# Kernel tuning notes

Hardware: AMD Instinct MI355X
Metric: run time of the kernel (lower is better)

## Reference

```python
import jax, jax.numpy as jnp
import numpy as np

B, E, H, W, P, C = 2, 256, 192, 192, 16, 80
GRIDS = (40, 36, 24, 16, 12)
L = len(GRIDS)
MASK_W, CLS_W, ALPHA, GAMMA, EPS = 3.0, 1.0, 0.25, 2.0, 1e-4


def setup_inputs() -> dict:
    key = jax.random.key(0)
    ks = jax.random.split(key, 32)
    inp = {"mask_out": jax.random.normal(ks[0], (B, E, H, W), jnp.float32)}
    for i, g in enumerate(GRIDS):
        inp[f"kernel_l{i}"] = jax.random.normal(ks[1 + i], (B, g, g, E), jnp.float32) * 0.05
        inp[f"cate_l{i}"] = jax.random.uniform(ks[6 + i], (B, g, g, C), jnp.float32)
        inp[f"pos_l{i}"] = jax.random.randint(ks[11 + i], (B, P), 0, g * g, dtype=jnp.int32)
        inp[f"cate_t_l{i}"] = jax.random.randint(ks[16 + i], (B, g, g), -1, C, dtype=jnp.int32)
    # binary instance masks, image-major layout [B, L, P, H, W]
    inp["mask_targets"] = (jax.random.uniform(ks[21], (B, L, P, H, W)) > 0.9).astype(jnp.float32)
    return inp


def _forward(mask_out, kernels, cates, mask_targets, pos_idxs, cate_ts):
    # --- dynamic 1x1 conv: gather positive kernels and apply as batched matmul ---
    preds = []
    for kl, pl in zip(kernels, pos_idxs):
        g2 = kl.shape[1] * kl.shape[2]
        kflat = kl.reshape(B, g2, E)
        kp = jnp.take_along_axis(kflat, pl[:, :, None], axis=1)  # [B, P, E]
        preds.append(jnp.einsum('bpe,behw->bphw', kp, mask_out))  # F.conv2d 1x1
    preds = jnp.stack(preds)  # [L, B, P, H, W]  (level-major, matches torch cat order)

    # --- dice loss ---
    mp = jax.nn.sigmoid(preds).reshape(L * B * P, H * W)
    # NOTE: original code concatenates targets image-major (img, level) while preds
    # are level-major (level, img); we reproduce that pairing faithfully.
    mt = mask_targets.reshape(B * L * P, H * W)
    a = jnp.sum(mp * mt, axis=1)
    b = jnp.sum(mp * mp, axis=1)
    c = jnp.sum(mt * mt, axis=1)
    mask_loss = jnp.sum(1.0 - 2.0 * a / (b + c + 1e-4)) / (L * B * P)

    # --- focal loss on positive grid cells ---
    tgt = jnp.concatenate([t.reshape(-1) for t in cate_ts])            # [N]
    prd = jnp.concatenate([cl.reshape(-1, C) for cl in cates])          # [N, C]
    posm = (tgt > -1).astype(jnp.float32)
    p = jnp.clip(prd, EPS, 1.0 - EPS)
    gt = jax.nn.one_hot(jnp.clip(tgt, 0, C - 1), C, dtype=jnp.float32)
    af = jnp.where(gt == 1.0, ALPHA, 1.0 - ALPHA)
    pt = jnp.where(gt == 1.0, p, 1.0 - p)
    fw = af * (1.0 - pt) ** GAMMA
    ce = -(gt * jnp.log(p) + (1.0 - gt) * jnp.log(1.0 - p))
    cls_loss = jnp.sum(fw * ce * posm[:, None]) / jnp.sum(posm)

    return jnp.stack([MASK_W * mask_loss, CLS_W * cls_loss])  # [mask_loss, cls_loss]


def reference(mask_out, kernel_l0, kernel_l1, kernel_l2, kernel_l3, kernel_l4,
              cate_l0, cate_l1, cate_l2, cate_l3, cate_l4, mask_targets,
              pos_l0, pos_l1, pos_l2, pos_l3, pos_l4,
              cate_t_l0, cate_t_l1, cate_t_l2, cate_t_l3, cate_t_l4):
    return _forward(mask_out,
                    (kernel_l0, kernel_l1, kernel_l2, kernel_l3, kernel_l4),
                    (cate_l0, cate_l1, cate_l2, cate_l3, cate_l4),
                    mask_targets,
                    (pos_l0, pos_l1, pos_l2, pos_l3, pos_l4),
                    (cate_t_l0, cate_t_l1, cate_t_l2, cate_t_l3, cate_t_l4))
```

## Files before the change

### kernel.cpp

```cpp
#include <hip/hip_runtime.h>
#include <hip/hip_bf16.h>

namespace {

constexpr int kHW = 36864;

typedef __attribute__((ext_vector_type(8))) short bf16x8;
typedef __attribute__((ext_vector_type(4))) float f32x4;

__device__ __forceinline__ unsigned short f2bf(float x) {
  return __builtin_bit_cast(unsigned short, __float2bfloat16(x));
}
__device__ __forceinline__ float bf2f(unsigned short u) {
  return __builtin_bit_cast(float, (unsigned int)u << 16);
}

__device__ __forceinline__ float wave_sum(float v) {
#pragma unroll
  for (int off = 32; off; off >>= 1) v += __shfl_xor(v, off, 64);
  return v;
}

__global__ __launch_bounds__(256) void prep_kernel(
    const float* __restrict__ k0, const float* __restrict__ k1,
    const float* __restrict__ k2, const float* __restrict__ k3,
    const float* __restrict__ k4,
    const int* __restrict__ q0, const int* __restrict__ q1,
    const int* __restrict__ q2, const int* __restrict__ q3,
    const int* __restrict__ q4,
    unsigned short* __restrict__ kbf, float* __restrict__ acc) {
  const int bid = blockIdx.x;
  if (bid == 0) {
    for (int i = threadIdx.x; i < 482; i += 256) acc[i] = 0.f;
    return;
  }
  const int idx = bid - 1;
  const int b = idx / 80;
  const int row = idx - b * 80;
  if (threadIdx.x >= 128) return;
  const int l = row >> 4, p = row & 15;
  const float* kb[5] = {k0, k1, k2, k3, k4};
  const int* pb[5] = {q0, q1, q2, q3, q4};
  const int bg2[5] = {b * 1600, b * 1296, b * 576, b * 256, b * 144};
  const int pos = pb[l][b * 16 + p];
  const int ch = threadIdx.x * 2;
  const float2 kv = *(const float2*)(kb[l] + (size_t)(bg2[l] + pos) * 256 + ch);
  *(unsigned int*)&kbf[((size_t)b * 80 + row) * 256 + ch] =
      (unsigned int)f2bf(kv.x) | ((unsigned int)f2bf(kv.y) << 16);
}

template <int FUSED>
__global__ __launch_bounds__(256, 4) void gemm_kernel(
    const float* __restrict__ mask_out,
    const unsigned short* __restrict__ kbf,
    const float* __restrict__ mask_targets,
    unsigned short* __restrict__ predw,
    float* __restrict__ acc) {
  __shared__ float bufB[2][32][64];
  __shared__ float bred[4][240];

  const int bid = blockIdx.x;
  const int b = bid / 576;
  const int tile = bid - b * 576;
  const int px0 = tile * 64;
  const int lane = threadIdx.x & 63;
  const int wv = threadIdx.x >> 6;
  const int px16 = lane & 15;
  const int hi8 = (lane >> 4) * 8;
  const int pxl = px0 + wv * 16 + px16;

  const unsigned short* __restrict__ ka =
      kbf + ((size_t)b * 80 + px16) * 256 + hi8;

  const float* __restrict__ gstage = mask_out + (size_t)b * 256 * kHW +
                                     (size_t)(wv * 4 + (lane >> 4)) * kHW +
                                     px0 + (lane & 15) * 4;

#define STAGE(CUR, KS)                                                       \
  {                                                                          \
    const float* gs = gstage + (size_t)(KS)*32 * kHW;                        \
    __builtin_amdgcn_global_load_lds(                                        \
        (const __attribute__((address_space(1))) unsigned int*)gs,           \
        (__attribute__((address_space(3))) unsigned int*)&bufB[CUR][wv * 4]  \
            [0],                                                             \
        16, 0, 0);                                                           \
    __builtin_amdgcn_global_load_lds(                                        \
        (const __attribute__((address_space(1))) unsigned int*)(gs +         \
                                                                16 * kHW),   \
        (__attribute__((address_space(3))) unsigned int*)&bufB[CUR][wv * 4 + \
                                                                   16][0],   \
        16, 0, 0);                                                           \
  }

  f32x4 a5[5];
#pragma unroll
  for (int mt = 0; mt < 5; ++mt) a5[mt] = (f32x4){0.f, 0.f, 0.f, 0.f};

  STAGE(0, 0);
  __syncthreads();

#pragma unroll
  for (int ks = 0; ks < 8; ++ks) {
    if (ks + 1 < 8) STAGE((ks + 1) & 1, ks + 1);
    float fb[8];
#pragma unroll
    for (int j = 0; j < 8; ++j) fb[j] = bufB[ks & 1][hi8 + j][wv * 16 + px16];
    bf16x8 bb;
#pragma unroll
    for (int j = 0; j < 8; ++j) bb[j] = (short)f2bf(fb[j]);
#pragma unroll
    for (int mt = 0; mt < 5; ++mt) {
      const bf16x8 af = *(const bf16x8*)(ka + mt * 4096 + ks * 32);
      a5[mt] =
          __builtin_amdgcn_mfma_f32_16x16x32_bf16(af, bb, a5[mt], 0, 0, 0);
    }
    __syncthreads();
  }
#undef STAGE

  if constexpr (FUSED == 0) {
#pragma unroll
    for (int mt = 0; mt < 5; ++mt) {
#pragma unroll
      for (int j = 0; j < 4; ++j) {
        const int row80 = mt * 16 + (lane >> 4) * 4 + j;
        const int r = (row80 >> 4) * 32 + b * 16 + (row80 & 15);
        predw[(size_t)r * kHW + pxl] = f2bf(a5[mt][j]);
      }
    }
  } else {
#pragma unroll
    for (int mt = 0; mt < 5; ++mt) {
#pragma unroll
      for (int j = 0; j < 4; ++j) {
        const int row80 = mt * 16 + (lane >> 4) * 4 + j;
        const int r = (row80 >> 4) * 32 + b * 16 + (row80 & 15);
        const float mp = 1.f / (1.f + __expf(-a5[mt][j]));
        const float tv = mask_targets[(size_t)r * kHW + pxl];
        float av = mp * tv;
        float bv = mp * mp;
        float cv = tv;
#pragma unroll
        for (int m = 1; m <= 8; m <<= 1) {
          av += __shfl_xor(av, m, 64);
          bv += __shfl_xor(bv, m, 64);
          cv += __shfl_xor(cv, m, 64);
        }
        if (px16 == 0) {
          bred[wv][row80] = av;
          bred[wv][80 + row80] = bv;
          bred[wv][160 + row80] = cv;
        }
      }
    }
    __syncthreads();
    if (threadIdx.x < 240) {
      const int q = threadIdx.x / 80;
      const int row80 = threadIdx.x - q * 80;
      const int r = (row80 >> 4) * 32 + b * 16 + (row80 & 15);
      const float s = bred[0][threadIdx.x] + bred[1][threadIdx.x] +
                      bred[2][threadIdx.x] + bred[3][threadIdx.x];
      unsafeAtomicAdd(&acc[q * 160 + r], s);
    }
  }
}

__global__ __launch_bounds__(256) void dice_kernel(
    const unsigned short* __restrict__ predw,
    const float* __restrict__ mtg, float* __restrict__ acc) {
  const int r = blockIdx.x / 18;
  const int cb = blockIdx.x - r * 18;
  const int px = cb * 2048 + threadIdx.x * 8;
  const size_t base = (size_t)r * kHW + px;
  const bf16x8 p8 = *(const bf16x8*)&predw[base];
  const float4 t0 = *(const float4*)&mtg[base];
  const float4 t1 = *(const float4*)&mtg[base + 4];
  const float tv[8] = {t0.x, t0.y, t0.z, t0.w, t1.x, t1.y, t1.z, t1.w};
  float av = 0.f, bv = 0.f, cv = 0.f;
#pragma unroll
  for (int j = 0; j < 8; ++j) {
    const float x = bf2f((unsigned short)p8[j]);
    const float mp = 1.f / (1.f + __expf(-x));
    av = fmaf(mp, tv[j], av);
    bv = fmaf(mp, mp, bv);
    cv += tv[j];
  }
  av = wave_sum(av);
  bv = wave_sum(bv);
  cv = wave_sum(cv);
  __shared__ float st[12];
  const int w = threadIdx.x >> 6;
  if ((threadIdx.x & 63) == 0) {
    st[w] = av;
    st[4 + w] = bv;
    st[8 + w] = cv;
  }
  __syncthreads();
  if (threadIdx.x < 3) {
    const int q = threadIdx.x;
    unsafeAtomicAdd(&acc[q * 160 + r], st[q * 4] + st[q * 4 + 1] +
                                           st[q * 4 + 2] + st[q * 4 + 3]);
  }
}

__global__ __launch_bounds__(256) void focal_kernel(
    const float* __restrict__ c0, const float* __restrict__ c1,
    const float* __restrict__ c2, const float* __restrict__ c3,
    const float* __restrict__ c4,
    const int* __restrict__ t0, const int* __restrict__ t1,
    const int* __restrict__ t2, const int* __restrict__ t3,
    const int* __restrict__ t4,
    float* __restrict__ acc) {
  const int idx = blockIdx.x * 256 + threadIdx.x;
  const int n = idx / 20;
  const int cq = (idx - n * 20) * 4;
  int t;
  const float* crow;
  if (n < 3200) {
    t = t0[n]; crow = c0 + (size_t)n * 80;
  } else if (n < 5792) {
    const int o = n - 3200; t = t1[o]; crow = c1 + (size_t)o * 80;
  } else if (n < 6944) {
    const int o = n - 5792; t = t2[o]; crow = c2 + (size_t)o * 80;
  } else if (n < 7456) {
    const int o = n - 6944; t = t3[o]; crow = c3 + (size_t)o * 80;
  } else {
    const int o = n - 7456; t = t4[o]; crow = c4 + (size_t)o * 80;
  }
  float term = 0.f, np = 0.f;
  if (t > -1) {
    const float4 pv4 = *(const float4*)&crow[cq];
    const float pvs[4] = {pv4.x, pv4.y, pv4.z, pv4.w};
#pragma unroll
    for (int j = 0; j < 4; ++j) {
      float pv = fminf(fmaxf(pvs[j], 1e-4f), 1.f - 1e-4f);
      const bool gm = (cq + j == t);
      const float af = gm ? 0.25f : 0.75f;
      const float pt = gm ? pv : 1.f - pv;
      const float om = 1.f - pt;
      term = fmaf(af * om * om, -__logf(pt), term);
    }
    if (cq == 0) np = 1.f;
  }
  term = wave_sum(term);
  np = wave_sum(np);
  __shared__ float st[8];
  const int wid = threadIdx.x >> 6;
  if ((threadIdx.x & 63) == 0) {
    st[wid] = term;
    st[4 + wid] = np;
  }
  __syncthreads();
  if (threadIdx.x == 0) {
    unsafeAtomicAdd(&acc[480], st[0] + st[1] + st[2] + st[3]);
    unsafeAtomicAdd(&acc[481], st[4] + st[5] + st[6] + st[7]);
  }
}

__global__ __launch_bounds__(64) void finalize_kernel(
    const float* __restrict__ acc, float* __restrict__ out) {
  const int tid = threadIdx.x;
  float s = 0.f;
#pragma unroll
  for (int rr = 0; rr < 3; ++rr) {
    const int r = tid + rr * 64;
    if (r < 160) {
      const float a = acc[r];
      const float bb = acc[160 + r];
      const float cc = acc[320 + r];
      s += 1.f - 2.f * a / (bb + cc + 1e-4f);
    }
  }
  s = wave_sum(s);
  if (tid == 0) {
    out[0] = 3.0f * (s / 160.f);
    out[1] = acc[480] / acc[481];
  }
}

}

extern "C" void kernel_launch(void* const* d_in, const int* in_sizes, int n_in,
                              void* d_out, int out_size, void* d_ws,
                              size_t ws_size, hipStream_t stream) {
  const float* mask_out = (const float*)d_in[0];
  const float* k[5];
  const float* cc[5];
  const int* pp[5];
  const int* tt[5];
  for (int i = 0; i < 5; ++i) {
    k[i] = (const float*)d_in[1 + 4 * i];
    cc[i] = (const float*)d_in[2 + 4 * i];
    pp[i] = (const int*)d_in[3 + 4 * i];
    tt[i] = (const int*)d_in[4 + 4 * i];
  }
  const float* mt = (const float*)d_in[21];

  char* ws = (char*)d_ws;
  float* acc = (float*)ws;
  unsigned short* kbf = (unsigned short*)(ws + 4096);
  unsigned short* predw = (unsigned short*)(ws + 90112);
  const size_t need = 90112 + (size_t)160 * kHW * 2;
  float* out = (float*)d_out;

  hipLaunchKernelGGL(prep_kernel, dim3(161), dim3(256), 0, stream, k[0], k[1],
                     k[2], k[3], k[4], pp[0], pp[1], pp[2], pp[3], pp[4], kbf,
                     acc);
  if (ws_size >= need) {
    hipLaunchKernelGGL((gemm_kernel<0>), dim3(1152), dim3(256), 0, stream,
                       mask_out, kbf, mt, predw, acc);
    hipLaunchKernelGGL(dice_kernel, dim3(160 * 18), dim3(256), 0, stream,
                       predw, mt, acc);
  } else {
    hipLaunchKernelGGL((gemm_kernel<1>), dim3(1152), dim3(256), 0, stream,
                       mask_out, kbf, mt, predw, acc);
  }
  hipLaunchKernelGGL(focal_kernel, dim3(605), dim3(256), 0, stream, cc[0],
                     cc[1], cc[2], cc[3], cc[4], tt[0], tt[1], tt[2], tt[3],
                     tt[4], acc);
  hipLaunchKernelGGL(finalize_kernel, dim3(1), dim3(64), 0, stream, acc, out);
}
```

Before: 72.55 us.

## Load GEMM B operand directly into registers, dropping LDS double-buffering

Replaces the LDS double-buffered staging of mask_out (global_load_lds plus barriers) with direct per-lane global loads of all 64 values per thread into registers up front, then runs the MFMA loop with no synchronisation. The fused fallback path and its workspace size check are removed, so the non-fused GEMM plus dice kernel path always runs. Occupancy hints change from launch_bounds(256,4) to waves_per_eu(2,4) to make room for the extra registers. Each lane's loads are 4-byte strided loads with 64-byte contiguous runs per row, which may coalesce worse than the previous 16-byte LDS loads, and higher register pressure may lower occupancy.

```diff
diff --git a/kernel.cpp b/kernel.cpp
--- a/kernel.cpp
+++ b/kernel.cpp
@@ -49,16 +49,11 @@
       (unsigned int)f2bf(kv.x) | ((unsigned int)f2bf(kv.y) << 16);
 }
 
-template <int FUSED>
-__global__ __launch_bounds__(256, 4) void gemm_kernel(
-    const float* __restrict__ mask_out,
-    const unsigned short* __restrict__ kbf,
-    const float* __restrict__ mask_targets,
-    unsigned short* __restrict__ predw,
-    float* __restrict__ acc) {
-  __shared__ float bufB[2][32][64];
-  __shared__ float bred[4][240];
-
+__global__ __attribute__((amdgpu_flat_work_group_size(256, 256),
+                          amdgpu_waves_per_eu(2, 4)))
+void gemm_store_kernel(const float* __restrict__ mask_out,
+                       const unsigned short* __restrict__ kbf,
+                       unsigned short* __restrict__ predw) {
   const int bid = blockIdx.x;
   const int b = bid / 576;
   const int tile = bid - b * 576;
@@ -69,98 +64,48 @@
   const int hi8 = (lane >> 4) * 8;
   const int pxl = px0 + wv * 16 + px16;
 
+  const float* __restrict__ mo =
+      mask_out + (size_t)b * 256 * kHW + (size_t)hi8 * kHW + pxl;
+
+  float br[8][8];
+#pragma unroll
+  for (int ks = 0; ks < 8; ++ks)
+#pragma unroll
+    for (int j = 0; j < 8; ++j)
+      br[ks][j] = mo[(size_t)(ks * 32 + j) * kHW];
+
+#pragma unroll
+  for (int ks = 0; ks < 8; ++ks)
+#pragma unroll
+    for (int j = 0; j < 8; ++j) asm volatile("" : "+v"(br[ks][j]));
+
   const unsigned short* __restrict__ ka =
       kbf + ((size_t)b * 80 + px16) * 256 + hi8;
 
-  const float* __restrict__ gstage = mask_out + (size_t)b * 256 * kHW +
-                                     (size_t)(wv * 4 + (lane >> 4)) * kHW +
-                                     px0 + (lane & 15) * 4;
-
-#define STAGE(CUR, KS)                                                       \
-  {                                                                          \
-    const float* gs = gstage + (size_t)(KS)*32 * kHW;                        \
-    __builtin_amdgcn_global_load_lds(                                        \
-        (const __attribute__((address_space(1))) unsigned int*)gs,           \
-        (__attribute__((address_space(3))) unsigned int*)&bufB[CUR][wv * 4]  \
-            [0],                                                             \
-        16, 0, 0);                                                           \
-    __builtin_amdgcn_global_load_lds(                                        \
-        (const __attribute__((address_space(1))) unsigned int*)(gs +         \
-                                                                16 * kHW),   \
-        (__attribute__((address_space(3))) unsigned int*)&bufB[CUR][wv * 4 + \
-                                                                   16][0],   \
-        16, 0, 0);                                                           \
-  }
-
   f32x4 a5[5];
 #pragma unroll
   for (int mt = 0; mt < 5; ++mt) a5[mt] = (f32x4){0.f, 0.f, 0.f, 0.f};
 
-  STAGE(0, 0);
-  __syncthreads();
-
 #pragma unroll
   for (int ks = 0; ks < 8; ++ks) {
-    if (ks + 1 < 8) STAGE((ks + 1) & 1, ks + 1);
-    float fb[8];
-#pragma unroll
-    for (int j = 0; j < 8; ++j) fb[j] = bufB[ks & 1][hi8 + j][wv * 16 + px16];
     bf16x8 bb;
 #pragma unroll
-    for (int j = 0; j < 8; ++j) bb[j] = (short)f2bf(fb[j]);
+    for (int j = 0; j < 8; ++j) bb[j] = (short)f2bf(br[ks][j]);
 #pragma unroll
     for (int mt = 0; mt < 5; ++mt) {
       const bf16x8 af = *(const bf16x8*)(ka + mt * 4096 + ks * 32);
       a5[mt] =
           __builtin_amdgcn_mfma_f32_16x16x32_bf16(af, bb, a5[mt], 0, 0, 0);
     }
-    __syncthreads();
-  }
-#undef STAGE
-
-  if constexpr (FUSED == 0) {
-#pragma unroll
-    for (int mt = 0; mt < 5; ++mt) {
-#pragma unroll
-      for (int j = 0; j < 4; ++j) {
-        const int row80 = mt * 16 + (lane >> 4) * 4 + j;
-        const int r = (row80 >> 4) * 32 + b * 16 + (row80 & 15);
-        predw[(size_t)r * kHW + pxl] = f2bf(a5[mt][j]);
-      }
-    }
-  } else {
-#pragma unroll
-    for (int mt = 0; mt < 5; ++mt) {
-#pragma unroll
-      for (int j = 0; j < 4; ++j) {
-        const int row80 = mt * 16 + (lane >> 4) * 4 + j;
-        const int r = (row80 >> 4) * 32 + b * 16 + (row80 & 15);
-        const float mp = 1.f / (1.f + __expf(-a5[mt][j]));
-        const float tv = mask_targets[(size_t)r * kHW + pxl];
-        float av = mp * tv;
-        float bv = mp * mp;
-        float cv = tv;
-#pragma unroll
-        for (int m = 1; m <= 8; m <<= 1) {
-          av += __shfl_xor(av, m, 64);
-          bv += __shfl_xor(bv, m, 64);
-          cv += __shfl_xor(cv, m, 64);
-        }
-        if (px16 == 0) {
-          bred[wv][row80] = av;
-          bred[wv][80 + row80] = bv;
-          bred[wv][160 + row80] = cv;
-        }
-      }
-    }
-    __syncthreads();
-    if (threadIdx.x < 240) {
-      const int q = threadIdx.x / 80;
-      const int row80 = threadIdx.x - q * 80;
+  }
+
+#pragma unroll
+  for (int mt = 0; mt < 5; ++mt) {
+#pragma unroll
+    for (int j = 0; j < 4; ++j) {
+      const int row80 = mt * 16 + (lane >> 4) * 4 + j;
       const int r = (row80 >> 4) * 32 + b * 16 + (row80 & 15);
-      const float s = bred[0][threadIdx.x] + bred[1][threadIdx.x] +
-                      bred[2][threadIdx.x] + bred[3][threadIdx.x];
-      unsafeAtomicAdd(&acc[q * 160 + r], s);
+      predw[(size_t)r * kHW + pxl] = f2bf(a5[mt][j]);
     }
   }
 }
@@ -298,23 +243,17 @@
 
   char* ws = (char*)d_ws;
   float* acc = (float*)ws;
-  unsigned short* kbf = (unsigned short*)(ws + 4096);
+  unsigned short* kbf = (unsigned short*)(ws + 8192);
   unsigned short* predw = (unsigned short*)(ws + 90112);
-  const size_t need = 90112 + (size_t)160 * kHW * 2;
   float* out = (float*)d_out;
 
   hipLaunchKernelGGL(prep_kernel, dim3(161), dim3(256), 0, stream, k[0], k[1],
                      k[2], k[3], k[4], pp[0], pp[1], pp[2], pp[3], pp[4], kbf,
                      acc);
-  if (ws_size >= need) {
-    hipLaunchKernelGGL((gemm_kernel<0>), dim3(1152), dim3(256), 0, stream,
-                       mask_out, kbf, mt, predw, acc);
-    hipLaunchKernelGGL(dice_kernel, dim3(160 * 18), dim3(256), 0, stream,
-                       predw, mt, acc);
-  } else {
-    hipLaunchKernelGGL((gemm_kernel<1>), dim3(1152), dim3(256), 0, stream,
-                       mask_out, kbf, mt, predw, acc);
-  }
+  hipLaunchKernelGGL(gemm_store_kernel, dim3(1152), dim3(256), 0, stream,
+                     mask_out, kbf, predw);
+  hipLaunchKernelGGL(dice_kernel, dim3(160 * 18), dim3(256), 0, stream, predw,
+                     mt, acc);
   hipLaunchKernelGGL(focal_kernel, dim3(605), dim3(256), 0, stream, cc[0],
                      cc[1], cc[2], cc[3], cc[4], tt[0], tt[1], tt[2], tt[3],
                      tt[4], acc);
```

Result: slower. 74.55 us (+2.8%).
